# Kernel optimization log

Hardware: AMD Instinct MI355X
Metric: run time of the kernel (lower is better)

Reference implementation:

```python
import jax, jax.numpy as jnp
import numpy as np

N = 30000      # points
E = 400000     # edges
CIN = 16       # input point features
B = 4          # graphs in batch
H, W = 60, 80  # BEV grid


def _mlp_params(key, cin, cout):
    k1, k2 = jax.random.split(key)
    wa = jax.random.normal(k1, (cin, cout), jnp.float32) * np.float32(np.sqrt(2.0 / cin))
    wb = jax.random.normal(k2, (cout, cout), jnp.float32) * np.float32(np.sqrt(2.0 / cout))
    return wa, jnp.zeros((cout,), jnp.float32), wb, jnp.zeros((cout,), jnp.float32)


def setup_inputs() -> dict:
    key = jax.random.key(0)
    ks = jax.random.split(key, 8)
    x = jax.random.normal(ks[0], (N, CIN), jnp.float32)
    r = jax.random.uniform(ks[1], (N, 3), jnp.float32)
    Z = 1.0 + 9.0 * r[:, 2]
    X = (r[:, 0] - 0.5) * 1.2 * Z   # |X/Z| < 0.6 -> mostly inside image
    Y = (r[:, 1] - 0.5) * 0.9 * Z
    pos = jnp.stack([X, Y, Z], axis=1)
    edge_index = jax.random.randint(ks[2], (2, E), 0, N, jnp.int32)
    batch = jnp.sort(jax.random.randint(ks[3], (N,), 0, B, jnp.int32))
    K = jnp.array([[500.0, 0.0, 320.0], [0.0, 500.0, 240.0], [0.0, 0.0, 1.0]], jnp.float32)
    w11, b11, w12, b12 = _mlp_params(ks[4], CIN + 3, 64)
    w21, b21, w22, b22 = _mlp_params(ks[5], 64 + 3, 128)
    w31, b31, w32, b32 = _mlp_params(ks[6], 128 + 3, 256)
    return dict(x=x, pos=pos, K=K,
                w11=w11, b11=b11, w12=w12, b12=b12,
                w21=w21, b21=b21, w22=w22, b22=b22,
                w31=w31, b31=b31, w32=w32, b32=b32,
                edge_index=edge_index, batch=batch)


def _mlp(h, wa, ba, wb, bb):
    return jax.nn.relu(h @ wa + ba) @ wb + bb


def _pointnet_conv(feat, rel, src, dst, wa, ba, wb, bb):
    # PyG PointNetConv: msg = local_nn([x_j, pos_j - pos_i]); max-aggregate at target i
    msg = _mlp(jnp.concatenate([feat[src], rel], axis=1), wa, ba, wb, bb)
    agg = jax.ops.segment_max(msg, dst, num_segments=N)
    return jnp.where(jnp.isfinite(agg), agg, 0.0)  # empty segments -> 0 (PyG fill)


def _points_to_image(feat, pos, batch, K):
    X, Y, Z = pos[:, 0], pos[:, 1], pos[:, 2]
    u = ((K[0, 0] * X / Z + K[0, 2]) / 640.0 * W).astype(jnp.int32)  # trunc like .long()
    v = ((K[1, 1] * Y / Z + K[1, 2]) / 480.0 * H).astype(jnp.int32)
    mask = (u >= 0) & (u < W) & (v >= 0) & (v < H)
    idx = jnp.where(mask, batch * (H * W) + v * W + u, 0)
    contrib = feat * mask[:, None].astype(feat.dtype)
    flat = jnp.zeros((B * H * W, feat.shape[1]), feat.dtype).at[idx].add(contrib)
    return flat.reshape(B, H, W, feat.shape[1]).transpose(0, 3, 1, 2)


def reference(x, pos, K, w11, b11, w12, b12, w21, b21, w22, b22, w31, b31, w32, b32,
              edge_index, batch):
    src, dst = edge_index[0], edge_index[1]
    rel = pos[src] - pos[dst]
    h = _pointnet_conv(x, rel, src, dst, w11, b11, w12, b12)
    h = _pointnet_conv(h, rel, src, dst, w21, b21, w22, b22)
    h = _pointnet_conv(h, rel, src, dst, w31, b31, w32, b32)
    return _points_to_image(h, pos, batch, K)  # [B, 256, H, W]
```

## Files before the change

kernel.cpp:

```cpp
#include <hip/hip_runtime.h>
#include <math.h>

#define NN 30000
#define NE 400000

typedef _Float16 f16;
typedef _Float16 f16x8 __attribute__((ext_vector_type(8)));
typedef float f32x4 __attribute__((ext_vector_type(4)));

__device__ __forceinline__ void atomic_max_f(float* addr, float v) {
    if (v >= 0.0f) {
        atomicMax((int*)addr, __float_as_int(v));
    } else {
        atomicMin((unsigned int*)addr, __float_as_uint(v));
    }
}

__global__ __launch_bounds__(256) void fill_neg_inf(float* p, int n) {
    int i = blockIdx.x * blockDim.x + threadIdx.x;
    int stride = gridDim.x * blockDim.x;
    for (; i < n; i += stride) p[i] = -INFINITY;
}

__global__ __launch_bounds__(256) void hist_dst(const int* __restrict__ dst,
                                                int* __restrict__ counts) {
    int e = blockIdx.x * 256 + threadIdx.x;
    if (e < NE) atomicAdd(&counts[dst[e]], 1);
}

__global__ __launch_bounds__(1024) void scan_counts(const int* __restrict__ counts,
                                                    int* __restrict__ cursor) {
    __shared__ int lsum[1024];
    const int t = threadIdx.x;
    const int base = t * 30;
    int s = 0;
    for (int i = 0; i < 30; ++i) {
        int idx = base + i;
        if (idx < NN) s += counts[idx];
    }
    lsum[t] = s;
    __syncthreads();
    int acc = s;
    for (int off = 1; off < 1024; off <<= 1) {
        int v = (t >= off) ? lsum[t - off] : 0;
        __syncthreads();
        acc += v;
        lsum[t] = acc;
        __syncthreads();
    }
    int run = acc - s;
    for (int i = 0; i < 30; ++i) {
        int idx = base + i;
        if (idx < NN) { cursor[idx] = run; run += counts[idx]; }
    }
}

__global__ __launch_bounds__(256) void scatter_edges(const int* __restrict__ src,
                                                     const int* __restrict__ dst,
                                                     int* __restrict__ cursor,
                                                     int* __restrict__ srcS,
                                                     int* __restrict__ dstS) {
    int e = blockIdx.x * 256 + threadIdx.x;
    if (e >= NE) return;
    int d = dst[e];
    int p = atomicAdd(&cursor[d], 1);
    srcS[p] = src[e];
    dstS[p] = d;
}

template<int K, int N>
__global__ __launch_bounds__(256) void pack_w(const float* __restrict__ wsrc,
                                              f16* __restrict__ pB) {
    int f = blockIdx.x * 256 + threadIdx.x;
    if (f >= K * N) return;
    int j = f & 7;
    int l = (f >> 3) & 63;
    int rest = f >> 9;
    constexpr int KS = K / 32;
    int ks = rest % KS;
    int nt = rest / KS;
    int k = ks * 32 + ((l >> 4) << 3) + j;
    int n = nt * 16 + (l & 15);
    pB[f] = (f16)wsrc[k * N + n];
}

__global__ __launch_bounds__(256) void cast_f16(const float* __restrict__ w,
                                                f16* __restrict__ o, int n) {
    int i = blockIdx.x * 256 + threadIdx.x;
    if (i < n) o[i] = (f16)w[i];
}

template<int K, int COUT>
__global__ __launch_bounds__(256) void node_linear(const float* __restrict__ feat,
                                                   const float* __restrict__ wa,
                                                   const float* __restrict__ b,
                                                   f16* __restrict__ A) {
    constexpr int NPB = 8;
    constexpr int G   = 256 / COUT;
    constexpr int NPT = NPB / G;
    __shared__ float sf[NPB * K];
    const int node0 = blockIdx.x * NPB;
    for (int idx = threadIdx.x; idx < NPB * K; idx += 256) {
        float v = feat[node0 * K + idx];
        if (!isfinite(v)) v = 0.0f;
        sf[idx] = v;
    }
    __syncthreads();
    const int j  = threadIdx.x % COUT;
    const int g  = threadIdx.x / COUT;
    const int n0 = g * NPT;
    float acc[NPT];
#pragma unroll
    for (int i = 0; i < NPT; i++) acc[i] = 0.0f;
    for (int k = 0; k < K; k++) {
        float w = wa[k * COUT + j];
#pragma unroll
        for (int nn = 0; nn < NPT; nn++)
            acc[nn] = fmaf(sf[(n0 + nn) * K + k], w, acc[nn]);
    }
    const float bj = b[j];
#pragma unroll
    for (int nn = 0; nn < NPT; nn++)
        A[(size_t)(node0 + n0 + nn) * COUT + j] = (f16)(acc[nn] + bj);
}

template<int K, int C>
__global__ __launch_bounds__(256) void node_gemm(const float* __restrict__ feat,
                                                 const f16* __restrict__ pW,
                                                 const float* __restrict__ bias,
                                                 f16* __restrict__ A) {
    constexpr int NTW = C / 64;
    constexpr int KS  = K / 32;
    __shared__ __align__(16) unsigned char smem[64 * K * 2];
    const int tid = threadIdx.x;
    const int node0 = blockIdx.x * 64;

    {
        const int e = tid >> 2, p = tid & 3;
        const bool valid = (node0 + e) < NN;
        const float* frow = feat + (size_t)(node0 + e) * K;
#pragma unroll
        for (int ch = 0; ch < K / 32; ++ch) {
            const int j0 = (ch * 4 + p) * 8;
            f16x8 hv;
#pragma unroll
            for (int jj = 0; jj < 8; ++jj) {
                float v = valid ? frow[j0 + jj] : 0.0f;
                if (!isfinite(v)) v = 0.0f;
                hv[jj] = (f16)v;
            }
            *(f16x8*)(smem + e * (K * 2) + ((j0 * 2) ^ ((e & 7) << 4))) = hv;
        }
    }
    __syncthreads();

    const int w = tid >> 6, l = tid & 63, lr = l & 15, lg = l >> 4;
    f32x4 acc[4][NTW] = {};
#pragma unroll
    for (int ks = 0; ks < KS; ++ks) {
        f16x8 af[4];
#pragma unroll
        for (int m = 0; m < 4; ++m) {
            const int row = m * 16 + lr;
            af[m] = *(const f16x8*)(smem + row * (K * 2)
                     + (((ks * 32 + lg * 8) * 2) ^ ((row & 7) << 4)));
        }
#pragma unroll
        for (int nt = 0; nt < NTW; ++nt) {
            const int ntg = w * NTW + nt;
            f16x8 bf = *(const f16x8*)(pW + ((size_t)(ntg * KS + ks) * 64 + l) * 8);
#pragma unroll
            for (int m = 0; m < 4; ++m)
                acc[m][nt] = __builtin_amdgcn_mfma_f32_16x16x32_f16(af[m], bf, acc[m][nt], 0, 0, 0);
        }
    }
#pragma unroll
    for (int m = 0; m < 4; ++m)
#pragma unroll
        for (int nt = 0; nt < NTW; ++nt) {
            const int col = w * (C / 4) + nt * 16 + lr;
            const float bv = bias[col];
#pragma unroll
            for (int rr = 0; rr < 4; ++rr) {
                const int row = m * 16 + lg * 4 + rr;
                if (node0 + row < NN)
                    A[(size_t)(node0 + row) * C + col] = (f16)(acc[m][nt][rr] + bv);
            }
        }
}

template<int C>
__global__ __launch_bounds__(256) void edge_mfma(const f16* __restrict__ Ah,
                                                 const f16* __restrict__ warelh,
                                                 const f16* __restrict__ pB,
                                                 const float* __restrict__ bb,
                                                 const float* __restrict__ pos,
                                                 const int* __restrict__ srcS,
                                                 const int* __restrict__ dstS,
                                                 float* __restrict__ agg) {
    constexpr int TE  = 64;
    constexpr int NTW = C / 64;
    constexpr int KS  = C / 32;
    __shared__ __align__(16) unsigned char h1[TE * C * 2];
    __shared__ float s_rx[TE], s_ry[TE], s_rz[TE];
    __shared__ int s_src[TE], s_dst[TE];

    const int tid = threadIdx.x;
    const int nwg = gridDim.x;
    const int q = nwg >> 3, r = nwg & 7;
    const int xcd = blockIdx.x & 7, o = blockIdx.x >> 3;
    const int bid = (xcd < r ? xcd * (q + 1) : r * (q + 1) + (xcd - r) * q) + o;
    const int e0 = bid * TE;

    if (tid < TE) {
        int s = srcS[e0 + tid], d = dstS[e0 + tid];
        s_src[tid] = s; s_dst[tid] = d;
        s_rx[tid] = pos[3 * s + 0] - pos[3 * d + 0];
        s_ry[tid] = pos[3 * s + 1] - pos[3 * d + 1];
        s_rz[tid] = pos[3 * s + 2] - pos[3 * d + 2];
    }
    __syncthreads();

    {
        const int e = tid >> 2, p = tid & 3;
        const int s = s_src[e];
        const f16 rx = (f16)s_rx[e], ry = (f16)s_ry[e], rz = (f16)s_rz[e];
        const f16x8 rxv = {rx, rx, rx, rx, rx, rx, rx, rx};
        const f16x8 ryv = {ry, ry, ry, ry, ry, ry, ry, ry};
        const f16x8 rzv = {rz, rz, rz, rz, rz, rz, rz, rz};
        const f16* arow = Ah + (size_t)s * C;
#pragma unroll
        for (int ch = 0; ch < C / 32; ++ch) {
            const int j0 = (ch * 4 + p) * 8;
            f16x8 av = *(const f16x8*)(arow + j0);
            f16x8 w0 = *(const f16x8*)(warelh + j0);
            f16x8 w1 = *(const f16x8*)(warelh + C + j0);
            f16x8 w2 = *(const f16x8*)(warelh + 2 * C + j0);
            f16x8 hv = av + rxv * w0 + ryv * w1 + rzv * w2;
#pragma unroll
            for (int jj = 0; jj < 8; ++jj)
                hv[jj] = hv[jj] > (f16)0.f ? hv[jj] : (f16)0.f;
            *(f16x8*)(h1 + e * (C * 2) + ((j0 * 2) ^ ((e & 7) << 4))) = hv;
        }
    }
    __syncthreads();

    const int w = tid >> 6, l = tid & 63, lr = l & 15, lg = l >> 4;
    f32x4 acc[4][NTW] = {};
    f16x8 bfc[NTW], bfn[NTW];
#pragma unroll
    for (int nt = 0; nt < NTW; ++nt)
        bfc[nt] = *(const f16x8*)(pB + ((size_t)((w * NTW + nt) * KS) * 64 + l) * 8);
#pragma unroll
    for (int ks = 0; ks < KS; ++ks) {
        if (ks + 1 < KS) {
#pragma unroll
            for (int nt = 0; nt < NTW; ++nt)
                bfn[nt] = *(const f16x8*)(pB + ((size_t)((w * NTW + nt) * KS + ks + 1) * 64 + l) * 8);
        }
        f16x8 af[4];
#pragma unroll
        for (int m = 0; m < 4; ++m) {
            const int row = m * 16 + lr;
            af[m] = *(const f16x8*)(h1 + row * (C * 2)
                     + (((ks * 32 + lg * 8) * 2) ^ ((row & 7) << 4)));
        }
#pragma unroll
        for (int nt = 0; nt < NTW; ++nt)
#pragma unroll
            for (int m = 0; m < 4; ++m)
                acc[m][nt] = __builtin_amdgcn_mfma_f32_16x16x32_f16(af[m], bfc[nt], acc[m][nt], 0, 0, 0);
#pragma unroll
        for (int nt = 0; nt < NTW; ++nt) bfc[nt] = bfn[nt];
    }

    float bbv[NTW];
#pragma unroll
    for (int nt = 0; nt < NTW; ++nt) bbv[nt] = bb[w * (C / 4) + nt * 16 + lr];

    const int myd = s_dst[l];
    const int pd  = s_dst[l == 0 ? 0 : l - 1];
    unsigned long long m = __ballot((l == 0) || (myd != pd));

    while (m) {
        const int a = __builtin_ctzll(m);
        const unsigned long long m2 = m & (m - 1);
        const int b = m2 ? __builtin_ctzll(m2) : 64;
        m = m2;
        const int d = s_dst[a];
#pragma unroll
        for (int nt = 0; nt < NTW; ++nt) {
            float v = -INFINITY;
#pragma unroll
            for (int mm = 0; mm < 4; ++mm) {
                if (b <= mm * 16 || a >= mm * 16 + 16) continue;
#pragma unroll
                for (int rr = 0; rr < 4; ++rr) {
                    const int row = mm * 16 + lg * 4 + rr;
                    const bool in = (row >= a) && (row < b);
                    v = fmaxf(v, in ? acc[mm][nt][rr] : -INFINITY);
                }
            }
            v = fmaxf(v, __shfl_xor(v, 16, 64));
            v = fmaxf(v, __shfl_xor(v, 32, 64));
            if (lg == 0)
                atomic_max_f(&agg[(size_t)d * C + w * (C / 4) + nt * 16 + lr], v + bbv[nt]);
        }
    }
}

__global__ __launch_bounds__(256) void scatter_img(const float* __restrict__ feat,
                                                   const float* __restrict__ pos,
                                                   const float* __restrict__ Km,
                                                   const int* __restrict__ batch,
                                                   float* __restrict__ img) {
    const int n = blockIdx.x;
    const float X = pos[3 * n + 0], Y = pos[3 * n + 1], Z = pos[3 * n + 2];
    const float k00 = Km[0], k02 = Km[2], k11 = Km[4], k12 = Km[5];
    const int u = (int)((k00 * X / Z + k02) / 640.0f * 80.0f);
    const int v = (int)((k11 * Y / Z + k12) / 480.0f * 60.0f);
    if (u < 0 || u >= 80 || v < 0 || v >= 60) return;
    const int p = (batch[n] * 60 + v) * 80 + u;
    const int c = threadIdx.x;
    float val = feat[(size_t)n * 256 + c];
    if (!isfinite(val)) val = 0.0f;
    atomicAdd(img + (size_t)p * 256 + c, val);
}

__global__ __launch_bounds__(256) void transpose_img(const float* __restrict__ img,
                                                     float* __restrict__ out) {
    __shared__ float tile[32][33];
    const int b = blockIdx.z;
    const int p0 = blockIdx.x * 32, c0 = blockIdx.y * 32;
    const float* src = img + (size_t)b * 4800 * 256;
    float* dst = out + (size_t)b * 256 * 4800;
    const int tx = threadIdx.x & 31, ty = threadIdx.x >> 5;
#pragma unroll
    for (int i = 0; i < 32; i += 8)
        tile[ty + i][tx] = src[(size_t)(p0 + ty + i) * 256 + c0 + tx];
    __syncthreads();
#pragma unroll
    for (int i = 0; i < 32; i += 8)
        dst[(size_t)(c0 + ty + i) * 4800 + p0 + tx] = tile[tx][ty + i];
}

extern "C" void kernel_launch(void* const* d_in, const int* in_sizes, int n_in,
                              void* d_out, int out_size, void* d_ws, size_t ws_size,
                              hipStream_t stream) {
    const float* x   = (const float*)d_in[0];
    const float* pos = (const float*)d_in[1];
    const float* Km  = (const float*)d_in[2];
    const float* w11 = (const float*)d_in[3];
    const float* b11 = (const float*)d_in[4];
    const float* w12 = (const float*)d_in[5];
    const float* b12 = (const float*)d_in[6];
    const float* w21 = (const float*)d_in[7];
    const float* b21 = (const float*)d_in[8];
    const float* w22 = (const float*)d_in[9];
    const float* b22 = (const float*)d_in[10];
    const float* w31 = (const float*)d_in[11];
    const float* b31 = (const float*)d_in[12];
    const float* w32 = (const float*)d_in[13];
    const float* b32 = (const float*)d_in[14];
    const int* edge  = (const int*)d_in[15];
    const int* batch = (const int*)d_in[16];
    const int* srcp = edge;
    const int* dstp = edge + NE;
    float* out = (float*)d_out;

    float* aggA  = (float*)d_ws;
    float* aggB  = aggA + (size_t)NN * 256;
    f16*   Ah    = (f16*)(aggB + (size_t)NN * 256);
    int*   srcS  = (int*)(Ah + (size_t)NN * 256);
    int*   dstS  = srcS + NE;
    int*   counts = dstS + NE;
    int*   cursor = counts + NN;
    f16*   pW1   = (f16*)(cursor + NN);
    f16*   pW2   = pW1 + 64 * 64;
    f16*   pW3   = pW2 + 128 * 128;
    f16*   pW2n  = pW3 + 256 * 256;
    f16*   pW3n  = pW2n + 64 * 128;
    f16*   wr1   = pW3n + 128 * 256;
    f16*   wr2   = wr1 + 3 * 64;
    f16*   wr3   = wr2 + 3 * 128;

    hipMemsetAsync(counts, 0, NN * sizeof(int), stream);
    hist_dst<<<(NE + 255) / 256, 256, 0, stream>>>(dstp, counts);
    scan_counts<<<1, 1024, 0, stream>>>(counts, cursor);
    scatter_edges<<<(NE + 255) / 256, 256, 0, stream>>>(srcp, dstp, cursor, srcS, dstS);

    pack_w<64, 64><<<(64 * 64 + 255) / 256, 256, 0, stream>>>(w12, pW1);
    pack_w<128, 128><<<(128 * 128 + 255) / 256, 256, 0, stream>>>(w22, pW2);
    pack_w<256, 256><<<(256 * 256 + 255) / 256, 256, 0, stream>>>(w32, pW3);
    pack_w<64, 128><<<(64 * 128 + 255) / 256, 256, 0, stream>>>(w21, pW2n);
    pack_w<128, 256><<<(128 * 256 + 255) / 256, 256, 0, stream>>>(w31, pW3n);
    cast_f16<<<1, 256, 0, stream>>>(w11 + 16 * 64, wr1, 3 * 64);
    cast_f16<<<2, 256, 0, stream>>>(w21 + 64 * 128, wr2, 3 * 128);
    cast_f16<<<3, 256, 0, stream>>>(w31 + 128 * 256, wr3, 3 * 256);

    node_linear<16, 64><<<NN / 8, 256, 0, stream>>>(x, w11, b11, Ah);
    fill_neg_inf<<<512, 256, 0, stream>>>(aggB, NN * 64);
    edge_mfma<64><<<NE / 64, 256, 0, stream>>>(Ah, wr1, pW1, b12,
                                               pos, srcS, dstS, aggB);
    node_gemm<64, 128><<<(NN + 63) / 64, 256, 0, stream>>>(aggB, pW2n, b21, Ah);
    fill_neg_inf<<<512, 256, 0, stream>>>(aggA, NN * 128);
    edge_mfma<128><<<NE / 64, 256, 0, stream>>>(Ah, wr2, pW2, b22,
                                                pos, srcS, dstS, aggA);
    node_gemm<128, 256><<<(NN + 63) / 64, 256, 0, stream>>>(aggA, pW3n, b31, Ah);
    fill_neg_inf<<<512, 256, 0, stream>>>(aggB, NN * 256);
    edge_mfma<256><<<NE / 64, 256, 0, stream>>>(Ah, wr3, pW3, b32,
                                                pos, srcS, dstS, aggB);
    hipMemsetAsync(aggA, 0, (size_t)4 * 4800 * 256 * sizeof(float), stream);
    scatter_img<<<NN, 256, 0, stream>>>(aggB, pos, Km, batch, aggA);
    transpose_img<<<dim3(150, 8, 4), 256, 0, stream>>>(aggA, out);
}
```

Baseline: 440.5 us.

## Gather source rows straight into LDS and fuse rel-pos ReLU into MFMA loop

The edge kernel now gathers each source node's precomputed A row into LDS with global_load_lds (async direct-to-LDS, swizzled slots) instead of loading it to registers, computing ReLU and storing it. The rel-pos term and ReLU are applied on the fly when MFMA A fragments are read, with the rel weights staged once in LDS. The B-fragment register double-buffering is removed and B is loaded per k-step. This is meant to cut VGPR traffic and one LDS write pass, at the cost of redoing the elementwise work in the MMA loop (each wave repeats it for its own column tiles) and exposing B-load latency.

```diff
diff --git a/kernel.cpp b/kernel.cpp
--- a/kernel.cpp
+++ b/kernel.cpp
@@ -6,7 +6,17 @@
 
 typedef _Float16 f16;
 typedef _Float16 f16x8 __attribute__((ext_vector_type(8)));
+typedef _Float16 f16x4 __attribute__((ext_vector_type(4)));
 typedef float f32x4 __attribute__((ext_vector_type(4)));
+
+__device__ __forceinline__ void gload_lds16(const void* g, void* lds) {
+    __builtin_amdgcn_global_load_lds(
+        reinterpret_cast<const __attribute__((address_space(1))) unsigned int*>(
+            reinterpret_cast<uintptr_t>(g)),
+        reinterpret_cast<__attribute__((address_space(3))) unsigned int*>(
+            reinterpret_cast<uintptr_t>(lds)),
+        16, 0, 0);
+}
 
 __device__ __forceinline__ void atomic_max_f(float* addr, float v) {
     if (v >= 0.0f) {
@@ -201,8 +211,11 @@
     constexpr int TE  = 64;
     constexpr int NTW = C / 64;
     constexpr int KS  = C / 32;
-    __shared__ __align__(16) unsigned char h1[TE * C * 2];
-    __shared__ float s_rx[TE], s_ry[TE], s_rz[TE];
+    constexpr int CPR = C / 8;
+    constexpr int LOGCPR = (C == 256) ? 5 : (C == 128 ? 4 : 3);
+    __shared__ __align__(16) unsigned char A_lds[TE * C * 2];
+    __shared__ __align__(16) f16 s_warel[3 * C];
+    __shared__ __align__(16) f16 s_rel[TE][4];
     __shared__ int s_src[TE], s_dst[TE];
 
     const int tid = threadIdx.x;
@@ -215,63 +228,60 @@
     if (tid < TE) {
         int s = srcS[e0 + tid], d = dstS[e0 + tid];
         s_src[tid] = s; s_dst[tid] = d;
-        s_rx[tid] = pos[3 * s + 0] - pos[3 * d + 0];
-        s_ry[tid] = pos[3 * s + 1] - pos[3 * d + 1];
-        s_rz[tid] = pos[3 * s + 2] - pos[3 * d + 2];
-    }
+        s_rel[tid][0] = (f16)(pos[3 * s + 0] - pos[3 * d + 0]);
+        s_rel[tid][1] = (f16)(pos[3 * s + 1] - pos[3 * d + 1]);
+        s_rel[tid][2] = (f16)(pos[3 * s + 2] - pos[3 * d + 2]);
+        s_rel[tid][3] = (f16)0.f;
+    }
+    for (int i = tid; i < 3 * C / 8; i += 256)
+        ((f16x8*)s_warel)[i] = ((const f16x8*)warelh)[i];
     __syncthreads();
 
     {
-        const int e = tid >> 2, p = tid & 3;
-        const int s = s_src[e];
-        const f16 rx = (f16)s_rx[e], ry = (f16)s_ry[e], rz = (f16)s_rz[e];
-        const f16x8 rxv = {rx, rx, rx, rx, rx, rx, rx, rx};
-        const f16x8 ryv = {ry, ry, ry, ry, ry, ry, ry, ry};
-        const f16x8 rzv = {rz, rz, rz, rz, rz, rz, rz, rz};
-        const f16* arow = Ah + (size_t)s * C;
-#pragma unroll
-        for (int ch = 0; ch < C / 32; ++ch) {
-            const int j0 = (ch * 4 + p) * 8;
-            f16x8 av = *(const f16x8*)(arow + j0);
-            f16x8 w0 = *(const f16x8*)(warelh + j0);
-            f16x8 w1 = *(const f16x8*)(warelh + C + j0);
-            f16x8 w2 = *(const f16x8*)(warelh + 2 * C + j0);
-            f16x8 hv = av + rxv * w0 + ryv * w1 + rzv * w2;
+        unsigned char* base = A_lds + ((tid & 192) << 4);
+#pragma unroll
+        for (int i = 0; i < C / 32; ++i) {
+            const int g    = i * 256 + tid;
+            const int row  = g >> LOGCPR;
+            const int slot = g & (CPR - 1);
+            const f16* ga = Ah + (size_t)s_src[row] * C + ((slot ^ (row & 7)) << 3);
+            gload_lds16(ga, base + i * 4096);
+        }
+    }
+    __syncthreads();
+
+    const int w = tid >> 6, l = tid & 63, lr = l & 15, lg = l >> 4;
+    f16x4 rv[4];
+#pragma unroll
+    for (int m = 0; m < 4; ++m)
+        rv[m] = *(const f16x4*)&s_rel[m * 16 + lr][0];
+
+    f32x4 acc[4][NTW] = {};
+#pragma unroll
+    for (int ks = 0; ks < KS; ++ks) {
+        const int co = ks * 32 + lg * 8;
+        f16x8 w0 = *(const f16x8*)(s_warel + co);
+        f16x8 w1 = *(const f16x8*)(s_warel + C + co);
+        f16x8 w2 = *(const f16x8*)(s_warel + 2 * C + co);
+        f16x8 af[4];
+#pragma unroll
+        for (int m = 0; m < 4; ++m) {
+            const int row = m * 16 + lr;
+            f16x8 av = *(const f16x8*)(A_lds + row * (2 * C)
+                        + (((ks * 4 + lg) ^ (row & 7)) << 4));
+            f16x8 hv = av + rv[m][0] * w0 + rv[m][1] * w1 + rv[m][2] * w2;
 #pragma unroll
             for (int jj = 0; jj < 8; ++jj)
                 hv[jj] = hv[jj] > (f16)0.f ? hv[jj] : (f16)0.f;
-            *(f16x8*)(h1 + e * (C * 2) + ((j0 * 2) ^ ((e & 7) << 4))) = hv;
-        }
-    }
-    __syncthreads();
-
-    const int w = tid >> 6, l = tid & 63, lr = l & 15, lg = l >> 4;
-    f32x4 acc[4][NTW] = {};
-    f16x8 bfc[NTW], bfn[NTW];
-#pragma unroll
-    for (int nt = 0; nt < NTW; ++nt)
-        bfc[nt] = *(const f16x8*)(pB + ((size_t)((w * NTW + nt) * KS) * 64 + l) * 8);
-#pragma unroll
-    for (int ks = 0; ks < KS; ++ks) {
-        if (ks + 1 < KS) {
-#pragma unroll
-            for (int nt = 0; nt < NTW; ++nt)
-                bfn[nt] = *(const f16x8*)(pB + ((size_t)((w * NTW + nt) * KS + ks + 1) * 64 + l) * 8);
-        }
-        f16x8 af[4];
-#pragma unroll
-        for (int m = 0; m < 4; ++m) {
-            const int row = m * 16 + lr;
-            af[m] = *(const f16x8*)(h1 + row * (C * 2)
-                     + (((ks * 32 + lg * 8) * 2) ^ ((row & 7) << 4)));
-        }
-#pragma unroll
-        for (int nt = 0; nt < NTW; ++nt)
+            af[m] = hv;
+        }
+#pragma unroll
+        for (int nt = 0; nt < NTW; ++nt) {
+            f16x8 bf = *(const f16x8*)(pB + ((size_t)((w * NTW + nt) * KS + ks) * 64 + l) * 8);
 #pragma unroll
             for (int m = 0; m < 4; ++m)
-                acc[m][nt] = __builtin_amdgcn_mfma_f32_16x16x32_f16(af[m], bfc[nt], acc[m][nt], 0, 0, 0);
-#pragma unroll
-        for (int nt = 0; nt < NTW; ++nt) bfc[nt] = bfn[nt];
+                acc[m][nt] = __builtin_amdgcn_mfma_f32_16x16x32_f16(af[m], bf, acc[m][nt], 0, 0, 0);
+        }
     }
 
     float bbv[NTW];
```

After: 500.3 us. 13.6% more time.
